# Optimization experiments

Hardware: AMD Instinct MI355X
Metric: run time of the kernel (lower is better)

The kernel has to match this reference:

```python
import jax, jax.numpy as jnp
import numpy as np

DIM = 256
HEADS = 8
HEAD_DIM = DIM // HEADS
WS = (2, 8, 8)  # window size (t, h, w)
N = WS[0] * WS[1] * WS[2]  # 128 tokens per window
SCALE = HEAD_DIM ** -0.5
MLP_HIDDEN = int(DIM * 2.0)
EPS = 1e-5

# static relative-position index table [N, N]
def _rel_pos_index():
    coords = np.stack(np.meshgrid(np.arange(WS[0]), np.arange(WS[1]), np.arange(WS[2]), indexing='ij'))
    cf = coords.reshape(3, -1)
    rel = cf[:, :, None] - cf[:, None, :]
    rel = rel.transpose(1, 2, 0).copy()
    rel[..., 0] += WS[0] - 1
    rel[..., 1] += WS[1] - 1
    rel[..., 2] += WS[2] - 1
    rel[..., 0] *= (2 * WS[1] - 1) * (2 * WS[2] - 1)
    rel[..., 1] *= (2 * WS[2] - 1)
    return rel.sum(-1)

REL_IDX = jnp.asarray(_rel_pos_index())  # [N, N] int
TABLE_SIZE = (2 * WS[0] - 1) * (2 * WS[1] - 1) * (2 * WS[2] - 1)  # 675


def layernorm(x, g, b):
    m = jnp.mean(x, axis=-1, keepdims=True)
    var = jnp.mean(jnp.square(x - m), axis=-1, keepdims=True)
    return (x - m) * jax.lax.rsqrt(var + EPS) * g + b


def window_partition(x):
    B, T, H, W, C = x.shape
    x = x.reshape(B, T // WS[0], WS[0], H // WS[1], WS[1], W // WS[2], WS[2], C)
    x = x.transpose(0, 1, 3, 5, 2, 4, 6, 7)
    return x.reshape(-1, N, C)


def window_reverse(wins, B, T, H, W):
    C = wins.shape[-1]
    x = wins.reshape(B, T // WS[0], H // WS[1], W // WS[2], WS[0], WS[1], WS[2], C)
    x = x.transpose(0, 1, 4, 2, 5, 3, 6, 7)
    return x.reshape(B, T, H, W, C)


def setup_inputs() -> dict:
    key = jax.random.key(0)
    ks = jax.random.split(key, 20)
    B, T, H, W = 2, 8, 64, 64
    f = lambda k, s, sc=0.02: jax.random.normal(k, s, dtype=jnp.float32) * sc
    return {
        'q': jax.random.normal(ks[0], (B, T, H, W, DIM), dtype=jnp.float32),
        'k': jax.random.normal(ks[1], (B, T, H, W, DIM), dtype=jnp.float32),
        'v': jax.random.normal(ks[2], (B, T, H, W, DIM), dtype=jnp.float32),
        'gq': jnp.ones((DIM,), jnp.float32), 'bq': jnp.zeros((DIM,), jnp.float32),
        'gk': jnp.ones((DIM,), jnp.float32), 'bk': jnp.zeros((DIM,), jnp.float32),
        'gv': jnp.ones((DIM,), jnp.float32), 'bv': jnp.zeros((DIM,), jnp.float32),
        'bias_table': f(ks[3], (TABLE_SIZE, HEADS)),
        'proj_w': f(ks[4], (DIM, DIM)), 'proj_b': jnp.zeros((DIM,), jnp.float32),
        'g2': jnp.ones((DIM,), jnp.float32), 'b2': jnp.zeros((DIM,), jnp.float32),
        'mw1': f(ks[5], (MLP_HIDDEN, DIM)), 'mb1': jnp.zeros((MLP_HIDDEN,), jnp.float32),
        'mw2': f(ks[6], (DIM, MLP_HIDDEN)), 'mb2': jnp.zeros((DIM,), jnp.float32),
    }


def reference(q, k, v, gq, bq, gk, bk, gv, bv, bias_table, proj_w, proj_b, g2, b2, mw1, mb1, mw2, mb2):
    B, T, H, W, C = q.shape
    shortcut = v
    qn = layernorm(q, gq, bq)
    kn = layernorm(k, gk, bk)
    vn = layernorm(v, gv, bv)
    # (dims divisible by window -> no padding needed)
    qw = window_partition(qn)  # [B_, N, C]
    kw = window_partition(kn)
    vw = window_partition(vn)
    B_ = qw.shape[0]
    to_heads = lambda t: t.reshape(B_, N, HEADS, HEAD_DIM).transpose(0, 2, 1, 3)  # [B_, h, N, d]
    qh, kh, vh = to_heads(qw), to_heads(kw), to_heads(vw)
    attn = jnp.einsum('bhnd,bhmd->bhnm', qh * SCALE, kh)
    bias = bias_table[REL_IDX]  # [N, N, heads]
    attn = attn + bias.transpose(2, 0, 1)[None]
    attn = jax.nn.softmax(attn, axis=-1)
    out = jnp.einsum('bhnm,bhmd->bhnd', attn, vh)
    out = out.transpose(0, 2, 1, 3).reshape(B_, N, C)
    out = out @ proj_w.T + proj_b
    x = window_reverse(out, B, T, H, W)
    x = shortcut + x
    h1 = layernorm(x, g2, b2)
    h1 = jax.nn.gelu(h1 @ mw1.T + mb1, approximate=False)
    x = x + (h1 @ mw2.T + mb2)
    return x
```

## Files before the change

### kernel.cpp

```cpp
#include <hip/hip_runtime.h>
#include <math.h>


typedef __attribute__((ext_vector_type(8))) short short8;
typedef __attribute__((ext_vector_type(4))) short shortx4;
typedef __attribute__((ext_vector_type(4))) float floatx4;

#define MFMA16(a, b, c) __builtin_amdgcn_mfma_f32_16x16x32_bf16((a), (b), (c), 0, 0, 0)
#define ATT_SCALE 0.17677669529663689f

__device__ __forceinline__ short f2bf(float f) {
  unsigned u = __float_as_uint(f);
  u += 0x7fffu + ((u >> 16) & 1u);
  return (short)(u >> 16);
}
__device__ __forceinline__ float bf2f(short s) {
  return __uint_as_float(((unsigned)(unsigned short)s) << 16);
}
__device__ __forceinline__ void gl2lds(const short* g, short* l) {
  __builtin_amdgcn_global_load_lds((const __attribute__((address_space(1))) void*)(g),
                                   (__attribute__((address_space(3))) void*)(l), 16, 0, 0);
}

__global__ void packP_kernel(const float* __restrict__ w, short* __restrict__ dst) {
  int idx = blockIdx.x * 256 + threadIdx.x;
  int r = (idx >> 6) & 255, us = (idx >> 3) & 7, e = idx & 7;
  int ph = idx >> 14;
  int u = us ^ (r & 7);
  dst[idx] = f2bf(w[r * 256 + ph * 64 + u * 8 + e]);
}
__global__ void pack1_kernel(const float* __restrict__ w, short* __restrict__ dst) {
  int idx = blockIdx.x * 256 + threadIdx.x;
  int hf = idx >> 16, ph = (idx >> 14) & 3, r = (idx >> 6) & 255, us = (idx >> 3) & 7, e = idx & 7;
  int u = us ^ (r & 7);
  dst[idx] = f2bf(w[(size_t)(hf * 256 + r) * 256 + ph * 64 + u * 8 + e]);
}
__global__ void pack2_kernel(const float* __restrict__ w, short* __restrict__ dst) {
  int idx = blockIdx.x * 256 + threadIdx.x;
  int ph = idx >> 14, r = (idx >> 6) & 255, us = (idx >> 3) & 7, e = idx & 7;
  int u = us ^ (r & 7);
  dst[idx] = f2bf(w[(size_t)r * 512 + ph * 64 + u * 8 + e]);
}

__global__ void biasprep_kernel(const float* __restrict__ table, short* __restrict__ biasPb) {
  int idx = blockIdx.x * 256 + threadIdx.x;
  int h = idx >> 14;
  int n = (idx >> 7) & 127;
  int lr = (idx >> 3) & 15;
  int c = idx & 7;
  int m = 16 * c + lr;
  int t1 = n >> 6, h1 = (n >> 3) & 7, w1 = n & 7;
  int t2 = m >> 6, h2 = (m >> 3) & 7, w2 = m & 7;
  int ridx = (t1 - t2 + 1) * 225 + (h1 - h2 + 7) * 15 + (w1 - w2 + 7);
  biasPb[idx] = f2bf(table[ridx * 8 + h]);
}

__global__ __launch_bounds__(256) void ln_qkv_kernel(
    const float* __restrict__ q, const float* __restrict__ k, const float* __restrict__ v,
    const float* __restrict__ gq, const float* __restrict__ bq,
    const float* __restrict__ gk, const float* __restrict__ bk,
    const float* __restrict__ gv, const float* __restrict__ bv,
    short* __restrict__ qw, short* __restrict__ kw, short* __restrict__ vw) {
  const int wv = threadIdx.x >> 6, l = threadIdx.x & 63;
  const int half = l >> 5, li = l & 31;
  const int tok = blockIdx.x * 8 + wv * 2 + half;
  const int which = blockIdx.y;
  const float* src = (which == 0) ? q : ((which == 1) ? k : v);
  const float* gg  = (which == 0) ? gq : ((which == 1) ? gk : gv);
  const float* bb  = (which == 0) ? bq : ((which == 1) ? bk : bv);
  short* dst       = (which == 0) ? qw : ((which == 1) ? kw : vw);

  float4 x0 = *(const float4*)(src + (size_t)tok * 256 + li * 8);
  float4 x1 = *(const float4*)(src + (size_t)tok * 256 + li * 8 + 4);
  float s1 = x0.x + x0.y + x0.z + x0.w + x1.x + x1.y + x1.z + x1.w;
  float s2 = x0.x * x0.x + x0.y * x0.y + x0.z * x0.z + x0.w * x0.w +
             x1.x * x1.x + x1.y * x1.y + x1.z * x1.z + x1.w * x1.w;
#pragma unroll
  for (int off = 1; off < 32; off <<= 1) {
    s1 += __shfl_xor(s1, off);
    s2 += __shfl_xor(s2, off);
  }
  float mean = s1 * (1.0f / 256.0f);
  float var = s2 * (1.0f / 256.0f) - mean * mean;
  float inv = rsqrtf(var + 1e-5f);

  int b_ = tok >> 15, rem = tok & 32767;
  int t = rem >> 12, hh = (rem >> 6) & 63, ww = rem & 63;
  int wi = ((b_ * 4 + (t >> 1)) * 8 + (hh >> 3)) * 8 + (ww >> 3);
  int n = ((t & 1) << 6) | ((hh & 7) << 3) | (ww & 7);

  float4 g0 = *(const float4*)(gg + li * 8);
  float4 g1 = *(const float4*)(gg + li * 8 + 4);
  float4 b0 = *(const float4*)(bb + li * 8);
  float4 b1 = *(const float4*)(bb + li * 8 + 4);
  short8 o;
  o[0] = f2bf((x0.x - mean) * inv * g0.x + b0.x);
  o[1] = f2bf((x0.y - mean) * inv * g0.y + b0.y);
  o[2] = f2bf((x0.z - mean) * inv * g0.z + b0.z);
  o[3] = f2bf((x0.w - mean) * inv * g0.w + b0.w);
  o[4] = f2bf((x1.x - mean) * inv * g1.x + b1.x);
  o[5] = f2bf((x1.y - mean) * inv * g1.y + b1.y);
  o[6] = f2bf((x1.z - mean) * inv * g1.z + b1.z);
  o[7] = f2bf((x1.w - mean) * inv * g1.w + b1.w);
  *(short8*)(dst + ((size_t)wi * 128 + n) * 256 + li * 8) = o;
}

__global__ __launch_bounds__(256, 4) void attn_kernel(
    const short* __restrict__ qw, const short* __restrict__ kw, const short* __restrict__ vw,
    const short* __restrict__ biasPb, short* __restrict__ ao) {
  __shared__ union SU {
    struct { short Qs[128][40]; short Ks[128][40]; } qk;
    short Ps[128 * 128];
  } su;
  __shared__ short Vt[32 * 128];

  const int wi = blockIdx.x, h = blockIdx.y, tid = threadIdx.x;
  const size_t base = (size_t)wi * 128 * 256 + h * 32;

#pragma unroll
  for (int i = 0; i < 2; ++i) {
    int idx = tid + 256 * i;
    int m = idx >> 2, c = idx & 3;
    *(short8*)&su.qk.Qs[m][c * 8] = *(const short8*)(qw + base + (size_t)m * 256 + c * 8);
    *(short8*)&su.qk.Ks[m][c * 8] = *(const short8*)(kw + base + (size_t)m * 256 + c * 8);
    short8 vv = *(const short8*)(vw + base + (size_t)m * 256 + c * 8);
#pragma unroll
    for (int e = 0; e < 8; ++e) {
      int d = c * 8 + e;
      Vt[d * 128 + (((m >> 3) ^ (d & 7)) << 3) + (m & 7)] = vv[e];
    }
  }
  __syncthreads();

  const int wvv = tid >> 6, l = tid & 63, lr = l & 15, g = l >> 4;
  const floatx4 zf = {0.f, 0.f, 0.f, 0.f};

  short8 aq0 = *(const short8*)&su.qk.Qs[32 * wvv + lr][g * 8];
  short8 aq1 = *(const short8*)&su.qk.Qs[32 * wvv + 16 + lr][g * 8];

  floatx4 s[2][8];
#pragma unroll
  for (int c = 0; c < 8; ++c) {
    short8 bk8 = *(const short8*)&su.qk.Ks[16 * c + lr][g * 8];
    s[0][c] = MFMA16(aq0, bk8, zf);
    s[1][c] = MFMA16(aq1, bk8, zf);
  }
  __syncthreads();

  const int lr7 = lr & 7;
#pragma unroll
  for (int r = 0; r < 2; ++r) {
#pragma unroll
    for (int j = 0; j < 4; ++j) {
      int n = 32 * wvv + 16 * r + 4 * g + j;
      short8 bv8 = *(const short8*)(biasPb + ((size_t)(h * 128 + n) * 16 + lr) * 8);
      float mx = -1e30f;
#pragma unroll
      for (int c = 0; c < 8; ++c) {
        float val = s[r][c][j] * ATT_SCALE + bf2f(bv8[c]);
        s[r][c][j] = val;
        mx = fmaxf(mx, val);
      }
#pragma unroll
      for (int off = 1; off < 16; off <<= 1) mx = fmaxf(mx, __shfl_xor(mx, off));
      float sum = 0.f;
#pragma unroll
      for (int c = 0; c < 8; ++c) {
        float e = __expf(s[r][c][j] - mx);
        s[r][c][j] = e;
        sum += e;
      }
#pragma unroll
      for (int off = 1; off < 16; off <<= 1) sum += __shfl_xor(sum, off);
      float invs = 1.0f / sum;
      int n7 = n & 7;
#pragma unroll
      for (int c = 0; c < 8; ++c) {
        int col = 16 * c + lr;
        su.Ps[n * 128 + (((col >> 3) ^ n7) << 3) + (col & 7)] = f2bf(s[r][c][j] * invs);
      }
    }
  }

  floatx4 o00 = zf, o01 = zf, o10 = zf, o11 = zf;
  const int ra0 = 32 * wvv + lr, ra1 = ra0 + 16;
#pragma unroll
  for (int ks = 0; ks < 4; ++ks) {
    int ulog = ks * 4 + g;
    short8 pa0 = *(const short8*)&su.Ps[ra0 * 128 + ((ulog ^ (ra0 & 7)) << 3)];
    short8 pa1 = *(const short8*)&su.Ps[ra1 * 128 + ((ulog ^ (ra1 & 7)) << 3)];
    short8 vb0 = *(const short8*)&Vt[lr * 128 + ((ulog ^ lr7) << 3)];
    short8 vb1 = *(const short8*)&Vt[(16 + lr) * 128 + ((ulog ^ lr7) << 3)];
    o00 = MFMA16(pa0, vb0, o00);
    o01 = MFMA16(pa0, vb1, o01);
    o10 = MFMA16(pa1, vb0, o10);
    o11 = MFMA16(pa1, vb1, o11);
  }

  __syncthreads();
  short* Ot = Vt;
#pragma unroll
  for (int j = 0; j < 4; ++j) {
    int n0 = 32 * wvv + 4 * g + j, n1 = n0 + 16;
    Ot[n0 * 32 + lr] = f2bf(o00[j]);
    Ot[n0 * 32 + 16 + lr] = f2bf(o01[j]);
    Ot[n1 * 32 + lr] = f2bf(o10[j]);
    Ot[n1 * 32 + 16 + lr] = f2bf(o11[j]);
  }
  __syncthreads();

  const int wbx = wi & 7, hbx = (wi >> 3) & 7, ttx = (wi >> 6) & 3, bbx = wi >> 8;
#pragma unroll
  for (int c = 0; c < 2; ++c) {
    int i = tid * 2 + c;
    int tok = i >> 2, ui = i & 3;
    int t0 = ttx * 2 + (tok >> 6), hh = hbx * 8 + ((tok >> 3) & 7), ww0 = wbx * 8 + (tok & 7);
    size_t sp = ((size_t)(bbx * 8 + t0) * 64 + hh) * 64 + ww0;
    *(short8*)(ao + sp * 256 + h * 32 + ui * 8) = *(const short8*)&Ot[tok * 32 + ui * 8];
  }
}

__global__ __launch_bounds__(256, 4) void projln_kernel(
    const short* __restrict__ ao, const short* __restrict__ wpk,
    const float* __restrict__ proj_b, const float* __restrict__ vin,
    const float* __restrict__ g2, const float* __restrict__ b2,
    short* __restrict__ xbf, short* __restrict__ xln) {
  __shared__ short WS[256 * 64];

  const int tid = threadIdx.x;
  const int w = tid >> 6, l = tid & 63, lr = l & 15, g = l >> 4;
  const floatx4 zf = {0.f, 0.f, 0.f, 0.f};
  const size_t token = (size_t)blockIdx.x * 64 + w * 16 + lr;

  floatx4 acc[16];
#pragma unroll
  for (int i = 0; i < 16; ++i) acc[i] = zf;

  short8 aA = *(const short8*)(ao + token * 256 + g * 8);
  short8 aB = *(const short8*)(ao + token * 256 + 32 + g * 8);
#pragma unroll
  for (int ph = 0; ph < 4; ++ph) {
    if (ph) __syncthreads();
    const short* src = wpk + ph * 16384;
#pragma unroll
    for (int i = 0; i < 8; ++i) {
      int ub = (i * 4 + w) * 64;
      gl2lds(src + (ub + l) * 8, WS + ub * 8);
    }
    __syncthreads();
    short8 nA, nB;
    if (ph < 3) {
      nA = *(const short8*)(ao + token * 256 + (ph + 1) * 64 + g * 8);
      nB = *(const short8*)(ao + token * 256 + (ph + 1) * 64 + 32 + g * 8);
    }
#pragma unroll
    for (int ct = 0; ct < 16; ++ct) {
      int rb = ct * 16 + lr;
      short8 b0 = *(const short8*)&WS[rb * 64 + ((g ^ (rb & 7)) << 3)];
      acc[ct] = MFMA16(b0, aA, acc[ct]);
      short8 b1 = *(const short8*)&WS[rb * 64 + (((4 + g) ^ (rb & 7)) << 3)];
      acc[ct] = MFMA16(b1, aB, acc[ct]);
    }
    aA = nA;
    aB = nB;
  }

  float s1 = 0.f, s2 = 0.f;
#pragma unroll
  for (int ct = 0; ct < 16; ++ct) {
    float4 pb = *(const float4*)(proj_b + ct * 16 + 4 * g);
    float4 vv = *(const float4*)(vin + token * 256 + ct * 16 + 4 * g);
#pragma unroll
    for (int j = 0; j < 4; ++j) {
      float val = acc[ct][j] + ((const float*)&pb)[j] + ((const float*)&vv)[j];
      acc[ct][j] = val;
      s1 += val;
      s2 += val * val;
    }
  }
  s1 += __shfl_xor(s1, 16); s1 += __shfl_xor(s1, 32);
  s2 += __shfl_xor(s2, 16); s2 += __shfl_xor(s2, 32);
  float mean = s1 * (1.0f / 256.0f);
  float var = s2 * (1.0f / 256.0f) - mean * mean;
  float inv = rsqrtf(var + 1e-5f);
#pragma unroll
  for (int ct = 0; ct < 16; ++ct) {
    shortx4 xo;
#pragma unroll
    for (int j = 0; j < 4; ++j) xo[j] = f2bf(acc[ct][j]);
    *(shortx4*)(xbf + token * 256 + ct * 16 + 4 * g) = xo;
  }
#pragma unroll
  for (int ct = 0; ct < 16; ++ct) {
    float4 gg = *(const float4*)(g2 + ct * 16 + 4 * g);
    float4 bb = *(const float4*)(b2 + ct * 16 + 4 * g);
    shortx4 lo;
#pragma unroll
    for (int j = 0; j < 4; ++j)
      lo[j] = f2bf((acc[ct][j] - mean) * inv * ((const float*)&gg)[j] + ((const float*)&bb)[j]);
    *(shortx4*)(xln + token * 256 + ct * 16 + 4 * g) = lo;
  }
}

__global__ __launch_bounds__(256, 4) void mlp1_kernel(
    const short* __restrict__ xln, const short* __restrict__ w1k,
    const float* __restrict__ mb1, short* __restrict__ h1) {
  __shared__ short WS[256 * 64];

  const int tid = threadIdx.x;
  const int w = tid >> 6, l = tid & 63, lr = l & 15, g = l >> 4;
  const int hf = blockIdx.y;
  const floatx4 zf = {0.f, 0.f, 0.f, 0.f};
  const size_t token = (size_t)blockIdx.x * 64 + w * 16 + lr;
  const short* wph = w1k + (size_t)hf * 65536;

  floatx4 acc[16];
#pragma unroll
  for (int i = 0; i < 16; ++i) acc[i] = zf;

  short8 aA = *(const short8*)(xln + token * 256 + g * 8);
  short8 aB = *(const short8*)(xln + token * 256 + 32 + g * 8);
#pragma unroll
  for (int ph = 0; ph < 4; ++ph) {
    if (ph) __syncthreads();
    const short* src = wph + ph * 16384;
#pragma unroll
    for (int i = 0; i < 8; ++i) {
      int ub = (i * 4 + w) * 64;
      gl2lds(src + (ub + l) * 8, WS + ub * 8);
    }
    __syncthreads();
    short8 nA, nB;
    if (ph < 3) {
      nA = *(const short8*)(xln + token * 256 + (ph + 1) * 64 + g * 8);
      nB = *(const short8*)(xln + token * 256 + (ph + 1) * 64 + 32 + g * 8);
    }
#pragma unroll
    for (int ct = 0; ct < 16; ++ct) {
      int rb = ct * 16 + lr;
      short8 b0 = *(const short8*)&WS[rb * 64 + ((g ^ (rb & 7)) << 3)];
      acc[ct] = MFMA16(b0, aA, acc[ct]);
      short8 b1 = *(const short8*)&WS[rb * 64 + (((4 + g) ^ (rb & 7)) << 3)];
      acc[ct] = MFMA16(b1, aB, acc[ct]);
    }
    aA = nA;
    aB = nB;
  }

#pragma unroll
  for (int ct = 0; ct < 16; ++ct) {
    float4 bb = *(const float4*)(mb1 + hf * 256 + ct * 16 + 4 * g);
    shortx4 ho;
#pragma unroll
    for (int j = 0; j < 4; ++j) {
      float xv = acc[ct][j] + ((const float*)&bb)[j];
      float yy = 1.5957691216057308f * (xv + 0.044715f * xv * xv * xv);
      float sg = 1.0f / (1.0f + __expf(-yy));
      ho[j] = f2bf(xv * sg);
    }
    *(shortx4*)(h1 + token * 512 + hf * 256 + ct * 16 + 4 * g) = ho;
  }
}

__global__ __launch_bounds__(256, 4) void mlp2_kernel(
    const short* __restrict__ h1, const short* __restrict__ w2k,
    const float* __restrict__ mb2, const short* __restrict__ xbf,
    float* __restrict__ out) {
  __shared__ short WS[256 * 64];

  const int tid = threadIdx.x;
  const int w = tid >> 6, l = tid & 63, lr = l & 15, g = l >> 4;
  const floatx4 zf = {0.f, 0.f, 0.f, 0.f};
  const size_t token = (size_t)blockIdx.x * 64 + w * 16 + lr;

  floatx4 acc[16];
#pragma unroll
  for (int i = 0; i < 16; ++i) acc[i] = zf;

  short8 aA = *(const short8*)(h1 + token * 512 + g * 8);
  short8 aB = *(const short8*)(h1 + token * 512 + 32 + g * 8);
#pragma unroll
  for (int ph = 0; ph < 8; ++ph) {
    if (ph) __syncthreads();
    const short* src = w2k + ph * 16384;
#pragma unroll
    for (int i = 0; i < 8; ++i) {
      int ub = (i * 4 + w) * 64;
      gl2lds(src + (ub + l) * 8, WS + ub * 8);
    }
    __syncthreads();
    short8 nA, nB;
    if (ph < 7) {
      nA = *(const short8*)(h1 + token * 512 + (ph + 1) * 64 + g * 8);
      nB = *(const short8*)(h1 + token * 512 + (ph + 1) * 64 + 32 + g * 8);
    }
#pragma unroll
    for (int ct = 0; ct < 16; ++ct) {
      int rb = ct * 16 + lr;
      short8 b0 = *(const short8*)&WS[rb * 64 + ((g ^ (rb & 7)) << 3)];
      acc[ct] = MFMA16(b0, aA, acc[ct]);
      short8 b1 = *(const short8*)&WS[rb * 64 + (((4 + g) ^ (rb & 7)) << 3)];
      acc[ct] = MFMA16(b1, aB, acc[ct]);
    }
    aA = nA;
    aB = nB;
  }

#pragma unroll
  for (int ct = 0; ct < 16; ++ct) {
    int oc = ct * 16 + 4 * g;
    float4 bb = *(const float4*)(mb2 + oc);
    shortx4 xb = *(const shortx4*)(xbf + token * 256 + oc);
    float4 o;
#pragma unroll
    for (int j = 0; j < 4; ++j)
      ((float*)&o)[j] = bf2f(xb[j]) + acc[ct][j] + ((const float*)&bb)[j];
    *(float4*)(out + token * 256 + oc) = o;
  }
}

extern "C" void kernel_launch(void* const* d_in, const int* in_sizes, int n_in,
                              void* d_out, int out_size, void* d_ws, size_t ws_size,
                              hipStream_t stream) {
  const float* q = (const float*)d_in[0];
  const float* k = (const float*)d_in[1];
  const float* v = (const float*)d_in[2];
  const float* gq = (const float*)d_in[3];
  const float* bq = (const float*)d_in[4];
  const float* gk = (const float*)d_in[5];
  const float* bk = (const float*)d_in[6];
  const float* gv = (const float*)d_in[7];
  const float* bv = (const float*)d_in[8];
  const float* bias_table = (const float*)d_in[9];
  const float* proj_w = (const float*)d_in[10];
  const float* proj_b = (const float*)d_in[11];
  const float* g2 = (const float*)d_in[12];
  const float* b2 = (const float*)d_in[13];
  const float* mw1 = (const float*)d_in[14];
  const float* mb1 = (const float*)d_in[15];
  const float* mw2 = (const float*)d_in[16];
  const float* mb2 = (const float*)d_in[17];

  char* ws = (char*)d_ws;
  short* qw = (short*)(ws + 0);
  short* kw = (short*)(ws + 33554432);
  short* vw = (short*)(ws + 67108864);
  short* ao = (short*)(ws + 100663296);
  short* xln = (short*)(ws + 0);
  short* xbf = (short*)(ws + 33554432);
  short* h1 = (short*)(ws + 67108864);
  short* wpk = (short*)(ws + 167772160);
  short* w1k = (short*)(ws + 167903232);
  short* w2k = (short*)(ws + 168165376);
  short* biasPb = (short*)(ws + 168427520);

  packP_kernel<<<256, 256, 0, stream>>>(proj_w, wpk);
  pack1_kernel<<<512, 256, 0, stream>>>(mw1, w1k);
  pack2_kernel<<<512, 256, 0, stream>>>(mw2, w2k);
  biasprep_kernel<<<512, 256, 0, stream>>>(bias_table, biasPb);

  ln_qkv_kernel<<<dim3(8192, 3), 256, 0, stream>>>(q, k, v, gq, bq, gk, bk, gv, bv, qw, kw, vw);

  attn_kernel<<<dim3(512, 8), 256, 0, stream>>>(qw, kw, vw, biasPb, ao);

  projln_kernel<<<1024, 256, 0, stream>>>(ao, wpk, proj_b, v, g2, b2, xbf, xln);

  mlp1_kernel<<<dim3(1024, 2), 256, 0, stream>>>(xln, w1k, mb1, h1);

  mlp2_kernel<<<1024, 256, 0, stream>>>(h1, w2k, mb2, xbf, (float*)d_out);
}
```

Baseline: 227.8 us.

## Fuse prep kernels, move window gather into attention, merge MLP1 halves

Merges the four weight and bias packing kernels into one launch to cut launch overhead. LayerNorm outputs are now written in natural token order and the attention kernel gathers window tokens itself, so the scattered writes leave ln_qkv. MLP1 now handles both hidden halves in a single block, loading each token's activations once into registers instead of twice across two grid rows. This lowers launch count and activation rereads, but gives a smaller MLP1 grid and higher register pressure.

```diff
diff --git a/kernel.cpp b/kernel.cpp
--- a/kernel.cpp
+++ b/kernel.cpp
@@ -22,37 +22,40 @@
                                    (__attribute__((address_space(3))) void*)(l), 16, 0, 0);
 }
 
-__global__ void packP_kernel(const float* __restrict__ w, short* __restrict__ dst) {
-  int idx = blockIdx.x * 256 + threadIdx.x;
-  int r = (idx >> 6) & 255, us = (idx >> 3) & 7, e = idx & 7;
-  int ph = idx >> 14;
-  int u = us ^ (r & 7);
-  dst[idx] = f2bf(w[r * 256 + ph * 64 + u * 8 + e]);
-}
-__global__ void pack1_kernel(const float* __restrict__ w, short* __restrict__ dst) {
-  int idx = blockIdx.x * 256 + threadIdx.x;
-  int hf = idx >> 16, ph = (idx >> 14) & 3, r = (idx >> 6) & 255, us = (idx >> 3) & 7, e = idx & 7;
-  int u = us ^ (r & 7);
-  dst[idx] = f2bf(w[(size_t)(hf * 256 + r) * 256 + ph * 64 + u * 8 + e]);
-}
-__global__ void pack2_kernel(const float* __restrict__ w, short* __restrict__ dst) {
-  int idx = blockIdx.x * 256 + threadIdx.x;
-  int ph = idx >> 14, r = (idx >> 6) & 255, us = (idx >> 3) & 7, e = idx & 7;
-  int u = us ^ (r & 7);
-  dst[idx] = f2bf(w[(size_t)r * 512 + ph * 64 + u * 8 + e]);
-}
-
-__global__ void biasprep_kernel(const float* __restrict__ table, short* __restrict__ biasPb) {
-  int idx = blockIdx.x * 256 + threadIdx.x;
-  int h = idx >> 14;
-  int n = (idx >> 7) & 127;
-  int lr = (idx >> 3) & 15;
-  int c = idx & 7;
-  int m = 16 * c + lr;
-  int t1 = n >> 6, h1 = (n >> 3) & 7, w1 = n & 7;
-  int t2 = m >> 6, h2 = (m >> 3) & 7, w2 = m & 7;
-  int ridx = (t1 - t2 + 1) * 225 + (h1 - h2 + 7) * 15 + (w1 - w2 + 7);
-  biasPb[idx] = f2bf(table[ridx * 8 + h]);
+__global__ void prep_kernel(const float* __restrict__ proj_w, const float* __restrict__ mw1,
+                            const float* __restrict__ mw2, const float* __restrict__ table,
+                            short* __restrict__ wpk, short* __restrict__ w1k,
+                            short* __restrict__ w2k, short* __restrict__ biasPb) {
+  int b = blockIdx.x, t = threadIdx.x;
+  if (b < 256) {
+    int idx = b * 256 + t;
+    int r = (idx >> 6) & 255, us = (idx >> 3) & 7, e = idx & 7;
+    int ph = idx >> 14;
+    int u = us ^ (r & 7);
+    wpk[idx] = f2bf(proj_w[r * 256 + ph * 64 + u * 8 + e]);
+  } else if (b < 768) {
+    int idx = (b - 256) * 256 + t;
+    int hf = idx >> 16, ph = (idx >> 14) & 3, r = (idx >> 6) & 255;
+    int us = (idx >> 3) & 7, e = idx & 7;
+    int u = us ^ (r & 7);
+    w1k[idx] = f2bf(mw1[(size_t)(hf * 256 + r) * 256 + ph * 64 + u * 8 + e]);
+  } else if (b < 1280) {
+    int idx = (b - 768) * 256 + t;
+    int ph = idx >> 14, r = (idx >> 6) & 255, us = (idx >> 3) & 7, e = idx & 7;
+    int u = us ^ (r & 7);
+    w2k[idx] = f2bf(mw2[(size_t)r * 512 + ph * 64 + u * 8 + e]);
+  } else {
+    int idx = (b - 1280) * 256 + t;
+    int h = idx >> 14;
+    int n = (idx >> 7) & 127;
+    int lr = (idx >> 3) & 15;
+    int c = idx & 7;
+    int m = 16 * c + lr;
+    int t1 = n >> 6, h1 = (n >> 3) & 7, w1 = n & 7;
+    int t2 = m >> 6, h2 = (m >> 3) & 7, w2 = m & 7;
+    int ridx = (t1 - t2 + 1) * 225 + (h1 - h2 + 7) * 15 + (w1 - w2 + 7);
+    biasPb[idx] = f2bf(table[ridx * 8 + h]);
+  }
 }
 
 __global__ __launch_bounds__(256) void ln_qkv_kernel(
@@ -84,11 +87,6 @@
   float var = s2 * (1.0f / 256.0f) - mean * mean;
   float inv = rsqrtf(var + 1e-5f);
 
-  int b_ = tok >> 15, rem = tok & 32767;
-  int t = rem >> 12, hh = (rem >> 6) & 63, ww = rem & 63;
-  int wi = ((b_ * 4 + (t >> 1)) * 8 + (hh >> 3)) * 8 + (ww >> 3);
-  int n = ((t & 1) << 6) | ((hh & 7) << 3) | (ww & 7);
-
   float4 g0 = *(const float4*)(gg + li * 8);
   float4 g1 = *(const float4*)(gg + li * 8 + 4);
   float4 b0 = *(const float4*)(bb + li * 8);
@@ -102,7 +100,7 @@
   o[5] = f2bf((x1.y - mean) * inv * g1.y + b1.y);
   o[6] = f2bf((x1.z - mean) * inv * g1.z + b1.z);
   o[7] = f2bf((x1.w - mean) * inv * g1.w + b1.w);
-  *(short8*)(dst + ((size_t)wi * 128 + n) * 256 + li * 8) = o;
+  *(short8*)(dst + (size_t)tok * 256 + li * 8) = o;
 }
 
 __global__ __launch_bounds__(256, 4) void attn_kernel(
@@ -115,15 +113,17 @@
   __shared__ short Vt[32 * 128];
 
   const int wi = blockIdx.x, h = blockIdx.y, tid = threadIdx.x;
-  const size_t base = (size_t)wi * 128 * 256 + h * 32;
+  const int b_ = wi >> 8, tt = (wi >> 6) & 3, hb = (wi >> 3) & 7, wb = wi & 7;
 
 #pragma unroll
   for (int i = 0; i < 2; ++i) {
     int idx = tid + 256 * i;
     int m = idx >> 2, c = idx & 3;
-    *(short8*)&su.qk.Qs[m][c * 8] = *(const short8*)(qw + base + (size_t)m * 256 + c * 8);
-    *(short8*)&su.qk.Ks[m][c * 8] = *(const short8*)(kw + base + (size_t)m * 256 + c * 8);
-    short8 vv = *(const short8*)(vw + base + (size_t)m * 256 + c * 8);
+    int t0 = tt * 2 + (m >> 6), hh = hb * 8 + ((m >> 3) & 7), ww0 = wb * 8 + (m & 7);
+    size_t sp = (((size_t)(b_ * 8 + t0) * 64 + hh) * 64 + ww0) * 256 + h * 32;
+    *(short8*)&su.qk.Qs[m][c * 8] = *(const short8*)(qw + sp + c * 8);
+    *(short8*)&su.qk.Ks[m][c * 8] = *(const short8*)(kw + sp + c * 8);
+    short8 vv = *(const short8*)(vw + sp + c * 8);
 #pragma unroll
     for (int e = 0; e < 8; ++e) {
       int d = c * 8 + e;
@@ -209,13 +209,12 @@
   }
   __syncthreads();
 
-  const int wbx = wi & 7, hbx = (wi >> 3) & 7, ttx = (wi >> 6) & 3, bbx = wi >> 8;
 #pragma unroll
   for (int c = 0; c < 2; ++c) {
     int i = tid * 2 + c;
     int tok = i >> 2, ui = i & 3;
-    int t0 = ttx * 2 + (tok >> 6), hh = hbx * 8 + ((tok >> 3) & 7), ww0 = wbx * 8 + (tok & 7);
-    size_t sp = ((size_t)(bbx * 8 + t0) * 64 + hh) * 64 + ww0;
+    int t0 = tt * 2 + (tok >> 6), hh = hb * 8 + ((tok >> 3) & 7), ww0 = wb * 8 + (tok & 7);
+    size_t sp = ((size_t)(b_ * 8 + t0) * 64 + hh) * 64 + ww0;
     *(short8*)(ao + sp * 256 + h * 32 + ui * 8) = *(const short8*)&Ot[tok * 32 + ui * 8];
   }
 }
@@ -309,56 +308,52 @@
 
   const int tid = threadIdx.x;
   const int w = tid >> 6, l = tid & 63, lr = l & 15, g = l >> 4;
-  const int hf = blockIdx.y;
   const floatx4 zf = {0.f, 0.f, 0.f, 0.f};
   const size_t token = (size_t)blockIdx.x * 64 + w * 16 + lr;
-  const short* wph = w1k + (size_t)hf * 65536;
-
-  floatx4 acc[16];
-#pragma unroll
-  for (int i = 0; i < 16; ++i) acc[i] = zf;
-
-  short8 aA = *(const short8*)(xln + token * 256 + g * 8);
-  short8 aB = *(const short8*)(xln + token * 256 + 32 + g * 8);
-#pragma unroll
-  for (int ph = 0; ph < 4; ++ph) {
-    if (ph) __syncthreads();
-    const short* src = wph + ph * 16384;
-#pragma unroll
-    for (int i = 0; i < 8; ++i) {
-      int ub = (i * 4 + w) * 64;
-      gl2lds(src + (ub + l) * 8, WS + ub * 8);
-    }
-    __syncthreads();
-    short8 nA, nB;
-    if (ph < 3) {
-      nA = *(const short8*)(xln + token * 256 + (ph + 1) * 64 + g * 8);
-      nB = *(const short8*)(xln + token * 256 + (ph + 1) * 64 + 32 + g * 8);
+
+  short8 a8[8];
+#pragma unroll
+  for (int s = 0; s < 8; ++s)
+    a8[s] = *(const short8*)(xln + token * 256 + s * 32 + g * 8);
+
+#pragma unroll
+  for (int hf = 0; hf < 2; ++hf) {
+    floatx4 acc[16];
+#pragma unroll
+    for (int i = 0; i < 16; ++i) acc[i] = zf;
+    const short* wph = w1k + (size_t)hf * 65536;
+#pragma unroll
+    for (int ph = 0; ph < 4; ++ph) {
+      if (hf | ph) __syncthreads();
+      const short* src = wph + ph * 16384;
+#pragma unroll
+      for (int i = 0; i < 8; ++i) {
+        int ub = (i * 4 + w) * 64;
+        gl2lds(src + (ub + l) * 8, WS + ub * 8);
+      }
+      __syncthreads();
+#pragma unroll
+      for (int ct = 0; ct < 16; ++ct) {
+        int rb = ct * 16 + lr;
+        short8 b0 = *(const short8*)&WS[rb * 64 + ((g ^ (rb & 7)) << 3)];
+        acc[ct] = MFMA16(b0, a8[2 * ph], acc[ct]);
+        short8 b1 = *(const short8*)&WS[rb * 64 + (((4 + g) ^ (rb & 7)) << 3)];
+        acc[ct] = MFMA16(b1, a8[2 * ph + 1], acc[ct]);
+      }
     }
 #pragma unroll
     for (int ct = 0; ct < 16; ++ct) {
-      int rb = ct * 16 + lr;
-      short8 b0 = *(const short8*)&WS[rb * 64 + ((g ^ (rb & 7)) << 3)];
-      acc[ct] = MFMA16(b0, aA, acc[ct]);
-      short8 b1 = *(const short8*)&WS[rb * 64 + (((4 + g) ^ (rb & 7)) << 3)];
-      acc[ct] = MFMA16(b1, aB, acc[ct]);
-    }
-    aA = nA;
-    aB = nB;
-  }
-
-#pragma unroll
-  for (int ct = 0; ct < 16; ++ct) {
-    float4 bb = *(const float4*)(mb1 + hf * 256 + ct * 16 + 4 * g);
-    shortx4 ho;
-#pragma unroll
-    for (int j = 0; j < 4; ++j) {
-      float xv = acc[ct][j] + ((const float*)&bb)[j];
-      float yy = 1.5957691216057308f * (xv + 0.044715f * xv * xv * xv);
-      float sg = 1.0f / (1.0f + __expf(-yy));
-      ho[j] = f2bf(xv * sg);
-    }
-    *(shortx4*)(h1 + token * 512 + hf * 256 + ct * 16 + 4 * g) = ho;
+      float4 bb = *(const float4*)(mb1 + hf * 256 + ct * 16 + 4 * g);
+      shortx4 ho;
+#pragma unroll
+      for (int j = 0; j < 4; ++j) {
+        float xv = acc[ct][j] + ((const float*)&bb)[j];
+        float yy = 1.5957691216057308f * (xv + 0.044715f * xv * xv * xv);
+        float sg = 1.0f / (1.0f + __expf(-yy));
+        ho[j] = f2bf(xv * sg);
+      }
+      *(shortx4*)(h1 + token * 512 + hf * 256 + ct * 16 + 4 * g) = ho;
+    }
   }
 }
 
@@ -454,10 +449,7 @@
   short* w2k = (short*)(ws + 168165376);
   short* biasPb = (short*)(ws + 168427520);
 
-  packP_kernel<<<256, 256, 0, stream>>>(proj_w, wpk);
-  pack1_kernel<<<512, 256, 0, stream>>>(mw1, w1k);
-  pack2_kernel<<<512, 256, 0, stream>>>(mw2, w2k);
-  biasprep_kernel<<<512, 256, 0, stream>>>(bias_table, biasPb);
+  prep_kernel<<<1792, 256, 0, stream>>>(proj_w, mw1, mw2, bias_table, wpk, w1k, w2k, biasPb);
 
   ln_qkv_kernel<<<dim3(8192, 3), 256, 0, stream>>>(q, k, v, gq, bq, gk, bk, gv, bv, qw, kw, vw);
 
@@ -465,7 +457,7 @@
 
   projln_kernel<<<1024, 256, 0, stream>>>(ao, wpk, proj_b, v, g2, b2, xbf, xln);
 
-  mlp1_kernel<<<dim3(1024, 2), 256, 0, stream>>>(xln, w1k, mb1, h1);
+  mlp1_kernel<<<1024, 256, 0, stream>>>(xln, w1k, mb1, h1);
 
   mlp2_kernel<<<1024, 256, 0, stream>>>(h1, w2k, mb2, xbf, (float*)d_out);
 }
```

New measurement: 239.7 us. +5.2%, slower.
